# Performance work log

Hardware: AMD Instinct MI355X
Metric: run time of the kernel (lower is better)

The kernel has to match this reference:

```python
import jax, jax.numpy as jnp
import numpy as np


def conv1x1(x, w, b):
    # x: [B,Cin,H,W], w: [Cout,Cin], b: [Cout]
    return jnp.einsum('bchw,oc->bohw', x, w) + b[None, :, None, None]


def setup_inputs() -> dict:
    key = jax.random.key(0)
    ks = jax.random.split(key, 10)
    B, Cm, C, H, W = 4, 6, 64, 64, 64
    map1 = jax.random.normal(ks[0], (B, Cm, H, W), jnp.float32)
    map2 = jax.random.normal(ks[1], (B, Cm, H, W), jnp.float32)
    feature_map = jax.random.normal(ks[2], (B, C, H, W), jnp.float32)
    # 1x1 conv params (kaiming-ish scale)
    wb = jax.random.normal(ks[3], (Cm, Cm), jnp.float32) / np.sqrt(Cm)
    bb = jnp.zeros((Cm,), jnp.float32)
    wc = jax.random.normal(ks[4], (Cm, Cm), jnp.float32) / np.sqrt(Cm)
    bc = jnp.zeros((Cm,), jnp.float32)
    wd = jax.random.normal(ks[5], (C, C), jnp.float32) / np.sqrt(C)
    bd = jnp.zeros((C,), jnp.float32)
    alpha = jnp.zeros((1,), jnp.float32)
    return {"map1": map1, "map2": map2, "feature_map": feature_map,
            "wb": wb, "bb": bb, "wc": wc, "bc": bc, "wd": wd, "bd": bd,
            "alpha": alpha}


def reference(map1, map2, feature_map, wb, bb, wc, bc, wd, bd, alpha):
    B, _, H, W = map1.shape
    N = H * W
    # conv1x1 projections, flatten spatial
    feat_b = conv1x1(map1, wb, bb).reshape(B, -1, N).transpose(0, 2, 1)  # [B,N,6]
    feat_c = conv1x1(map2, wc, bc).reshape(B, -1, N)                      # [B,6,N]
    attention_s = jax.nn.softmax(jnp.einsum('bnc,bcm->bnm', feat_b, feat_c), axis=-1)  # [B,N,N]
    feat_d = conv1x1(feature_map, wd, bd).reshape(B, -1, N)               # [B,C,N]
    # bmm with attention_s^T: out[b,c,n] = sum_m feat_d[b,c,m] * attn[b,n,m]
    feat_e = jnp.einsum('bcm,bnm->bcn', feat_d, attention_s).reshape(B, -1, H, W)
    return alpha * feat_e + feature_map
```

## Files before the change

kernel.cpp:

```cpp
#include <hip/hip_runtime.h>
#include <hip/hip_bf16.h>
#include <math.h>


#define BATCH 4
#define CMAP  6
#define CH    64
#define NSP   4096
#define TN    64
#define PSTR  72

typedef __attribute__((ext_vector_type(8))) short short8;
typedef __attribute__((ext_vector_type(4))) float f32x4;

#if __has_builtin(__builtin_amdgcn_exp2f)
#define EXP2(x) __builtin_amdgcn_exp2f(x)
#else
#define EXP2(x) exp2f(x)
#endif

__device__ __forceinline__ unsigned f2bf(float f) {
    unsigned u = __float_as_uint(f);
    return (u + 0x7fffu + ((u >> 16) & 1u)) >> 16;
}

#define INVLN2 1.44269504088896f
#define SHIFT_BF16 0xC238u
#define ONE_BF16   0x3F80u


__global__ void proj_kernel(const float* __restrict__ map1, const float* __restrict__ map2,
                            const float* __restrict__ fm,
                            const float* __restrict__ wb, const float* __restrict__ bb,
                            const float* __restrict__ wc, const float* __restrict__ bc,
                            const float* __restrict__ wd, const float* __restrict__ bd,
                            unsigned short* __restrict__ featq8,
                            unsigned short* __restrict__ featk8,
                            unsigned short* __restrict__ featdf)
{
    __shared__ unsigned short vfrag[2048];

    const int b    = blockIdx.z;
    const int half = blockIdx.y;
    const int lane = threadIdx.x & 63;
    const int og   = threadIdx.x >> 6;
    const int n    = blockIdx.x * 64 + lane;

    const int ht = lane >> 5;
    const int mm = lane & 31;
    const int q4 = mm >> 3, jj = mm & 7;
    const int cb_local = og >> 1;
    float vals[CH];
#pragma unroll
    for (int c = 0; c < CH; ++c)
        vals[c] = fm[(size_t)(b*CH + c)*NSP + n];
#pragma unroll
    for (int oi = 0; oi < 8; ++oi) {
        const int o = half*32 + og*8 + oi;
        float a = bd[o];
#pragma unroll
        for (int c = 0; c < CH; ++c)
            a = fmaf(vals[c], wd[o*CH + c], a);
        const int r = (og & 1)*8 + oi;
        vfrag[(ht*2 + cb_local)*512 + (q4*16 + r)*8 + jj] = (unsigned short)f2bf(a);
    }

    if (half == 0 && og == 0) {
        float v1[CMAP], v2[CMAP];
#pragma unroll
        for (int c = 0; c < CMAP; ++c) {
            v1[c] = map1[(size_t)(b*CMAP + c)*NSP + n];
            v2[c] = map2[(size_t)(b*CMAP + c)*NSP + n];
        }
        unsigned qv[CMAP], kv[CMAP];
#pragma unroll
        for (int o = 0; o < CMAP; ++o) {
            float a1 = bb[o], a2 = bc[o];
#pragma unroll
            for (int c = 0; c < CMAP; ++c) {
                a1 = fmaf(v1[c], wb[o*CMAP + c], a1);
                a2 = fmaf(v2[c], wc[o*CMAP + c], a2);
            }
            qv[o] = f2bf(a1 * INVLN2);
            kv[o] = f2bf(a2);
        }
        uint4 qw, kw;
        qw.x = qv[0] | (qv[1] << 16);
        qw.y = qv[2] | (qv[3] << 16);
        qw.z = qv[4] | (qv[5] << 16);
        qw.w = SHIFT_BF16;
        kw.x = kv[0] | (kv[1] << 16);
        kw.y = kv[2] | (kv[3] << 16);
        kw.z = kv[4] | (kv[5] << 16);
        kw.w = ONE_BF16;
        *(uint4*)&featq8[(size_t)(b*NSP + n)*8] = qw;
        *(uint4*)&featk8[(size_t)(b*NSP + n)*8] = kw;
    }

    __syncthreads();

    {
        const int tt = threadIdx.x;
        const uint4 d = *(const uint4*)&vfrag[tt*8];
        const int ht2 = tt >> 7, inner = tt & 127;
        const size_t off = (((size_t)(b*128 + blockIdx.x*2 + ht2)*4) + half*2)*512
                         + (size_t)inner*8;
        *(uint4*)&featdf[off] = d;
    }
}

__global__ __launch_bounds__(256, 2)
void attn_kernel(const unsigned short* __restrict__ featq8,
                 const unsigned short* __restrict__ featk8,
                 const unsigned short* __restrict__ featdf,
                 const float* __restrict__ fm, const float* __restrict__ alpha_p,
                 float* __restrict__ out)
{
    __shared__ unsigned short p_scr[2][4][16*PSTR];
    __shared__ float l_scr[4][16];

    const int b    = blockIdx.z;
    const int chh  = blockIdx.y;
    const int t    = threadIdx.x;
    const int lane = t & 63, w = t >> 6;
    const int row16 = lane & 15, quad = lane >> 4;
    const int n0w  = blockIdx.x * 64 + w * 16;

    short8 qf = {0,0,0,0,0,0,0,0};
    if (quad == 0)
        qf = *(const short8*)&featq8[(size_t)(b*NSP + n0w + row16)*8];

    const unsigned short* kbase = featk8 + ((size_t)b*NSP + row16)*8 + quad*8;
    const unsigned short* vfb = featdf + ((size_t)b*128*4)*512 + lane*8;
    const int cb0 = chh*2, cb1 = chh*2 + 1;

    const f32x4 zf = {0.f,0.f,0.f,0.f};
    f32x4 acc0 = zf, acc1 = zf;
    float lacc = 0.f;
    const int prow = row16 * PSTR;

#define PAM_DO(pwp, mb, sv)                                                     \
    {                                                                           \
        const float p0 = EXP2(sv[0]), p1 = EXP2(sv[1]);                         \
        const float p2 = EXP2(sv[2]), p3 = EXP2(sv[3]);                         \
        lacc += (p0 + p1) + (p2 + p3);                                          \
        uint2 pp;                                                               \
        pp.x = __builtin_amdgcn_perm(__float_as_uint(p1), __float_as_uint(p0), 0x07060302u); \
        pp.y = __builtin_amdgcn_perm(__float_as_uint(p3), __float_as_uint(p2), 0x07060302u); \
        *(uint2*)((pwp) + (mb)*16) = pp;                                        \
    }

    short8 k0 = *(const short8*)(kbase +  0*8);
    short8 k1 = *(const short8*)(kbase + 16*8);
    short8 k2 = *(const short8*)(kbase + 32*8);
    short8 k3 = *(const short8*)(kbase + 48*8);
    short8 vn0 = *(const short8*)(vfb + (size_t)(0*4 + cb0)*512);
    short8 vn1 = *(const short8*)(vfb + (size_t)(1*4 + cb0)*512);
    short8 vn2 = *(const short8*)(vfb + (size_t)(0*4 + cb1)*512);
    short8 vn3 = *(const short8*)(vfb + (size_t)(1*4 + cb1)*512);

    f32x4 s0 = __builtin_amdgcn_mfma_f32_16x16x32_bf16(k0, qf, zf, 0, 0, 0);
    f32x4 s1 = __builtin_amdgcn_mfma_f32_16x16x32_bf16(k1, qf, zf, 0, 0, 0);
    f32x4 s2 = __builtin_amdgcn_mfma_f32_16x16x32_bf16(k2, qf, zf, 0, 0, 0);
    f32x4 s3 = __builtin_amdgcn_mfma_f32_16x16x32_bf16(k3, qf, zf, 0, 0, 0);
    {
        unsigned short* pw = &p_scr[0][w][prow + quad*4];
        PAM_DO(pw, 0, s0) PAM_DO(pw, 1, s1) PAM_DO(pw, 2, s2) PAM_DO(pw, 3, s3)
    }
    k0 = *(const short8*)(kbase + (64 +  0)*8);
    k1 = *(const short8*)(kbase + (64 + 16)*8);
    k2 = *(const short8*)(kbase + (64 + 32)*8);
    k3 = *(const short8*)(kbase + (64 + 48)*8);
    short8 vv0 = vn0, vv1 = vn1, vv2 = vn2, vv3 = vn3;
    vn0 = *(const short8*)(vfb + (size_t)((2 + 0)*4 + cb0)*512);
    vn1 = *(const short8*)(vfb + (size_t)((2 + 1)*4 + cb0)*512);
    vn2 = *(const short8*)(vfb + (size_t)((2 + 0)*4 + cb1)*512);
    vn3 = *(const short8*)(vfb + (size_t)((2 + 1)*4 + cb1)*512);

#pragma unroll 2
    for (int tc = 1; tc < NSP/TN; ++tc) {
        const int par = tc & 1;

        s0 = __builtin_amdgcn_mfma_f32_16x16x32_bf16(k0, qf, zf, 0, 0, 0);
        s1 = __builtin_amdgcn_mfma_f32_16x16x32_bf16(k1, qf, zf, 0, 0, 0);
        s2 = __builtin_amdgcn_mfma_f32_16x16x32_bf16(k2, qf, zf, 0, 0, 0);
        s3 = __builtin_amdgcn_mfma_f32_16x16x32_bf16(k3, qf, zf, 0, 0, 0);

        const int kn = ((tc + 1) & (NSP/TN - 1)) * TN;
        const short8 k0n = *(const short8*)(kbase + (kn +  0)*8);
        const short8 k1n = *(const short8*)(kbase + (kn + 16)*8);
        const short8 k2n = *(const short8*)(kbase + (kn + 32)*8);
        const short8 k3n = *(const short8*)(kbase + (kn + 48)*8);

        const unsigned short* pr = &p_scr[par ^ 1][w][prow + quad*8];
        const short8 a0 = *(const short8*)pr;
        const short8 a1 = *(const short8*)(pr + 32);

        {
            unsigned short* pw = &p_scr[par][w][prow + quad*4];
            PAM_DO(pw, 0, s0) PAM_DO(pw, 1, s1) PAM_DO(pw, 2, s2) PAM_DO(pw, 3, s3)
        }

        acc0 = __builtin_amdgcn_mfma_f32_16x16x32_bf16(a0, vv0, acc0, 0, 0, 0);
        acc0 = __builtin_amdgcn_mfma_f32_16x16x32_bf16(a1, vv1, acc0, 0, 0, 0);
        acc1 = __builtin_amdgcn_mfma_f32_16x16x32_bf16(a0, vv2, acc1, 0, 0, 0);
        acc1 = __builtin_amdgcn_mfma_f32_16x16x32_bf16(a1, vv3, acc1, 0, 0, 0);

        vv0 = vn0; vv1 = vn1; vv2 = vn2; vv3 = vn3;
        const int vt = (tc + 1) & (NSP/TN - 1);
        vn0 = *(const short8*)(vfb + (size_t)((vt*2 + 0)*4 + cb0)*512);
        vn1 = *(const short8*)(vfb + (size_t)((vt*2 + 1)*4 + cb0)*512);
        vn2 = *(const short8*)(vfb + (size_t)((vt*2 + 0)*4 + cb1)*512);
        vn3 = *(const short8*)(vfb + (size_t)((vt*2 + 1)*4 + cb1)*512);

        k0 = k0n; k1 = k1n; k2 = k2n; k3 = k3n;
    }

    {
        const unsigned short* pr = &p_scr[1][w][prow + quad*8];
        const short8 a0 = *(const short8*)pr;
        const short8 a1 = *(const short8*)(pr + 32);
        acc0 = __builtin_amdgcn_mfma_f32_16x16x32_bf16(a0, vv0, acc0, 0, 0, 0);
        acc0 = __builtin_amdgcn_mfma_f32_16x16x32_bf16(a1, vv1, acc0, 0, 0, 0);
        acc1 = __builtin_amdgcn_mfma_f32_16x16x32_bf16(a0, vv2, acc1, 0, 0, 0);
        acc1 = __builtin_amdgcn_mfma_f32_16x16x32_bf16(a1, vv3, acc1, 0, 0, 0);
    }
#undef PAM_DO

    lacc += __shfl_xor(lacc, 16);
    lacc += __shfl_xor(lacc, 32);
    if (quad == 0) l_scr[w][row16] = lacc;
    const float4 lv = *(const float4*)&l_scr[w][quad*4];

    const float alpha = alpha_p[0];
    const float c0 = alpha / (lv.x + 1e-30f);
    const float c1 = alpha / (lv.y + 1e-30f);
    const float c2 = alpha / (lv.z + 1e-30f);
    const float c3 = alpha / (lv.w + 1e-30f);
#pragma unroll
    for (int cb = 0; cb < 2; ++cb) {
        const int ch = chh*32 + cb*16 + row16;
        const size_t base = (size_t)(b*CH + ch)*NSP + n0w + quad*4;
        const float4 f = *(const float4*)&fm[base];
        const f32x4 a = cb ? acc1 : acc0;
        float4 o;
        o.x = fmaf(c0, a[0], f.x);
        o.y = fmaf(c1, a[1], f.y);
        o.z = fmaf(c2, a[2], f.z);
        o.w = fmaf(c3, a[3], f.w);
        *(float4*)&out[base] = o;
    }
}

extern "C" void kernel_launch(void* const* d_in, const int* in_sizes, int n_in,
                              void* d_out, int out_size, void* d_ws, size_t ws_size,
                              hipStream_t stream)
{
    const float* map1  = (const float*)d_in[0];
    const float* map2  = (const float*)d_in[1];
    const float* fm    = (const float*)d_in[2];
    const float* wb    = (const float*)d_in[3];
    const float* bb    = (const float*)d_in[4];
    const float* wc    = (const float*)d_in[5];
    const float* bc    = (const float*)d_in[6];
    const float* wd    = (const float*)d_in[7];
    const float* bd    = (const float*)d_in[8];
    const float* alpha = (const float*)d_in[9];
    float* out = (float*)d_out;

    unsigned short* featq8 = (unsigned short*)d_ws;
    unsigned short* featk8 = featq8 + (size_t)BATCH*NSP*8;
    unsigned short* featdf = featk8 + (size_t)BATCH*NSP*8;

    proj_kernel<<<dim3(NSP/64, 2, BATCH), 256, 0, stream>>>(
        map1, map2, fm, wb, bb, wc, bc, wd, bd, featq8, featk8, featdf);
    attn_kernel<<<dim3(NSP/64, 2, BATCH), 256, 0, stream>>>(
        featq8, featk8, featdf, fm, alpha, out);
}
```

Before: 122.6 us.

## Compute softmax row sums via MFMA with ones and deepen QK pipeline

Replaces the per-lane VALU accumulation of exponentials and the shuffle/LDS reduction with two extra MFMAs per tile that multiply the bf16 P fragments by a ones vector, giving row sums directly in accumulator layout. It also restructures the software pipeline so QK scores for tile i are computed while tile i-1's scores are exponentiated, giving the MFMA latency a full iteration to hide. The row sum now comes from the bf16-rounded probabilities, which matches the numerator but changes rounding, and the extra MFMAs and live registers add matrix-unit work and register pressure.

```diff
diff --git a/kernel.cpp b/kernel.cpp
--- a/kernel.cpp
+++ b/kernel.cpp
@@ -8,6 +8,7 @@
 #define CH    64
 #define NSP   4096
 #define TN    64
+#define NT    (NSP/TN)
 #define PSTR  72
 
 typedef __attribute__((ext_vector_type(8))) short short8;
@@ -117,7 +118,6 @@
                  float* __restrict__ out)
 {
     __shared__ unsigned short p_scr[2][4][16*PSTR];
-    __shared__ float l_scr[4][16];
 
     const int b    = blockIdx.z;
     const int chh  = blockIdx.y;
@@ -130,92 +130,107 @@
     if (quad == 0)
         qf = *(const short8*)&featq8[(size_t)(b*NSP + n0w + row16)*8];
 
+    const short8 onesb = {(short)ONE_BF16,(short)ONE_BF16,(short)ONE_BF16,(short)ONE_BF16,
+                          (short)ONE_BF16,(short)ONE_BF16,(short)ONE_BF16,(short)ONE_BF16};
+
     const unsigned short* kbase = featk8 + ((size_t)b*NSP + row16)*8 + quad*8;
     const unsigned short* vfb = featdf + ((size_t)b*128*4)*512 + lane*8;
     const int cb0 = chh*2, cb1 = chh*2 + 1;
 
     const f32x4 zf = {0.f,0.f,0.f,0.f};
-    f32x4 acc0 = zf, acc1 = zf;
-    float lacc = 0.f;
+    f32x4 acc0 = zf, acc1 = zf, accL = zf;
     const int prow = row16 * PSTR;
 
 #define PAM_DO(pwp, mb, sv)                                                     \
     {                                                                           \
         const float p0 = EXP2(sv[0]), p1 = EXP2(sv[1]);                         \
         const float p2 = EXP2(sv[2]), p3 = EXP2(sv[3]);                         \
-        lacc += (p0 + p1) + (p2 + p3);                                          \
         uint2 pp;                                                               \
         pp.x = __builtin_amdgcn_perm(__float_as_uint(p1), __float_as_uint(p0), 0x07060302u); \
         pp.y = __builtin_amdgcn_perm(__float_as_uint(p3), __float_as_uint(p2), 0x07060302u); \
         *(uint2*)((pwp) + (mb)*16) = pp;                                        \
     }
 
-    short8 k0 = *(const short8*)(kbase +  0*8);
-    short8 k1 = *(const short8*)(kbase + 16*8);
-    short8 k2 = *(const short8*)(kbase + 32*8);
-    short8 k3 = *(const short8*)(kbase + 48*8);
-    short8 vn0 = *(const short8*)(vfb + (size_t)(0*4 + cb0)*512);
-    short8 vn1 = *(const short8*)(vfb + (size_t)(1*4 + cb0)*512);
-    short8 vn2 = *(const short8*)(vfb + (size_t)(0*4 + cb1)*512);
-    short8 vn3 = *(const short8*)(vfb + (size_t)(1*4 + cb1)*512);
-
-    f32x4 s0 = __builtin_amdgcn_mfma_f32_16x16x32_bf16(k0, qf, zf, 0, 0, 0);
-    f32x4 s1 = __builtin_amdgcn_mfma_f32_16x16x32_bf16(k1, qf, zf, 0, 0, 0);
-    f32x4 s2 = __builtin_amdgcn_mfma_f32_16x16x32_bf16(k2, qf, zf, 0, 0, 0);
-    f32x4 s3 = __builtin_amdgcn_mfma_f32_16x16x32_bf16(k3, qf, zf, 0, 0, 0);
-    {
+#define LOADK(dst, mt)                                                          \
+    dst##0 = *(const short8*)(kbase + ((mt)*TN +  0)*8);                        \
+    dst##1 = *(const short8*)(kbase + ((mt)*TN + 16)*8);                        \
+    dst##2 = *(const short8*)(kbase + ((mt)*TN + 32)*8);                        \
+    dst##3 = *(const short8*)(kbase + ((mt)*TN + 48)*8);
+
+#define LOADV(dst, vt)                                                          \
+    dst##0 = *(const short8*)(vfb + (size_t)(((vt)*2 + 0)*4 + cb0)*512);        \
+    dst##1 = *(const short8*)(vfb + (size_t)(((vt)*2 + 1)*4 + cb0)*512);        \
+    dst##2 = *(const short8*)(vfb + (size_t)(((vt)*2 + 0)*4 + cb1)*512);        \
+    dst##3 = *(const short8*)(vfb + (size_t)(((vt)*2 + 1)*4 + cb1)*512);
+
+    short8 kc0, kc1, kc2, kc3, kn0, kn1, kn2, kn3;
+    short8 vv0, vv1, vv2, vv3, vn0, vn1, vn2, vn3;
+    f32x4 sp0, sp1, sp2, sp3;
+
+    LOADK(kc, 0)
+    LOADV(vv, 0)
+    LOADV(vn, 1)
+
+    {
+        f32x4 a0 = __builtin_amdgcn_mfma_f32_16x16x32_bf16(kc0, qf, zf, 0, 0, 0);
+        f32x4 a1 = __builtin_amdgcn_mfma_f32_16x16x32_bf16(kc1, qf, zf, 0, 0, 0);
+        f32x4 a2 = __builtin_amdgcn_mfma_f32_16x16x32_bf16(kc2, qf, zf, 0, 0, 0);
+        f32x4 a3 = __builtin_amdgcn_mfma_f32_16x16x32_bf16(kc3, qf, zf, 0, 0, 0);
+        LOADK(kc, 1)
         unsigned short* pw = &p_scr[0][w][prow + quad*4];
-        PAM_DO(pw, 0, s0) PAM_DO(pw, 1, s1) PAM_DO(pw, 2, s2) PAM_DO(pw, 3, s3)
-    }
-    k0 = *(const short8*)(kbase + (64 +  0)*8);
-    k1 = *(const short8*)(kbase + (64 + 16)*8);
-    k2 = *(const short8*)(kbase + (64 + 32)*8);
-    k3 = *(const short8*)(kbase + (64 + 48)*8);
-    short8 vv0 = vn0, vv1 = vn1, vv2 = vn2, vv3 = vn3;
-    vn0 = *(const short8*)(vfb + (size_t)((2 + 0)*4 + cb0)*512);
-    vn1 = *(const short8*)(vfb + (size_t)((2 + 1)*4 + cb0)*512);
-    vn2 = *(const short8*)(vfb + (size_t)((2 + 0)*4 + cb1)*512);
-    vn3 = *(const short8*)(vfb + (size_t)((2 + 1)*4 + cb1)*512);
+        PAM_DO(pw, 0, a0) PAM_DO(pw, 1, a1) PAM_DO(pw, 2, a2) PAM_DO(pw, 3, a3)
+    }
+    sp0 = __builtin_amdgcn_mfma_f32_16x16x32_bf16(kc0, qf, zf, 0, 0, 0);
+    sp1 = __builtin_amdgcn_mfma_f32_16x16x32_bf16(kc1, qf, zf, 0, 0, 0);
+    sp2 = __builtin_amdgcn_mfma_f32_16x16x32_bf16(kc2, qf, zf, 0, 0, 0);
+    sp3 = __builtin_amdgcn_mfma_f32_16x16x32_bf16(kc3, qf, zf, 0, 0, 0);
+    LOADK(kc, 2)
 
 #pragma unroll 2
-    for (int tc = 1; tc < NSP/TN; ++tc) {
-        const int par = tc & 1;
-
-        s0 = __builtin_amdgcn_mfma_f32_16x16x32_bf16(k0, qf, zf, 0, 0, 0);
-        s1 = __builtin_amdgcn_mfma_f32_16x16x32_bf16(k1, qf, zf, 0, 0, 0);
-        s2 = __builtin_amdgcn_mfma_f32_16x16x32_bf16(k2, qf, zf, 0, 0, 0);
-        s3 = __builtin_amdgcn_mfma_f32_16x16x32_bf16(k3, qf, zf, 0, 0, 0);
-
-        const int kn = ((tc + 1) & (NSP/TN - 1)) * TN;
-        const short8 k0n = *(const short8*)(kbase + (kn +  0)*8);
-        const short8 k1n = *(const short8*)(kbase + (kn + 16)*8);
-        const short8 k2n = *(const short8*)(kbase + (kn + 32)*8);
-        const short8 k3n = *(const short8*)(kbase + (kn + 48)*8);
-
-        const unsigned short* pr = &p_scr[par ^ 1][w][prow + quad*8];
+    for (int i = 2; i < NT; ++i) {
+        const f32x4 t0 = __builtin_amdgcn_mfma_f32_16x16x32_bf16(kc0, qf, zf, 0, 0, 0);
+        const f32x4 t1 = __builtin_amdgcn_mfma_f32_16x16x32_bf16(kc1, qf, zf, 0, 0, 0);
+        const f32x4 t2 = __builtin_amdgcn_mfma_f32_16x16x32_bf16(kc2, qf, zf, 0, 0, 0);
+        const f32x4 t3 = __builtin_amdgcn_mfma_f32_16x16x32_bf16(kc3, qf, zf, 0, 0, 0);
+
+        const unsigned short* pr = &p_scr[i & 1][w][prow + quad*8];
         const short8 a0 = *(const short8*)pr;
         const short8 a1 = *(const short8*)(pr + 32);
 
+        LOADK(kn, i + 1)
+
         {
-            unsigned short* pw = &p_scr[par][w][prow + quad*4];
-            PAM_DO(pw, 0, s0) PAM_DO(pw, 1, s1) PAM_DO(pw, 2, s2) PAM_DO(pw, 3, s3)
+            unsigned short* pw = &p_scr[(i + 1) & 1][w][prow + quad*4];
+            PAM_DO(pw, 0, sp0) PAM_DO(pw, 1, sp1) PAM_DO(pw, 2, sp2) PAM_DO(pw, 3, sp3)
         }
 
         acc0 = __builtin_amdgcn_mfma_f32_16x16x32_bf16(a0, vv0, acc0, 0, 0, 0);
         acc0 = __builtin_amdgcn_mfma_f32_16x16x32_bf16(a1, vv1, acc0, 0, 0, 0);
         acc1 = __builtin_amdgcn_mfma_f32_16x16x32_bf16(a0, vv2, acc1, 0, 0, 0);
         acc1 = __builtin_amdgcn_mfma_f32_16x16x32_bf16(a1, vv3, acc1, 0, 0, 0);
+        accL = __builtin_amdgcn_mfma_f32_16x16x32_bf16(a0, onesb, accL, 0, 0, 0);
+        accL = __builtin_amdgcn_mfma_f32_16x16x32_bf16(a1, onesb, accL, 0, 0, 0);
 
         vv0 = vn0; vv1 = vn1; vv2 = vn2; vv3 = vn3;
-        const int vt = (tc + 1) & (NSP/TN - 1);
-        vn0 = *(const short8*)(vfb + (size_t)((vt*2 + 0)*4 + cb0)*512);
-        vn1 = *(const short8*)(vfb + (size_t)((vt*2 + 1)*4 + cb0)*512);
-        vn2 = *(const short8*)(vfb + (size_t)((vt*2 + 0)*4 + cb1)*512);
-        vn3 = *(const short8*)(vfb + (size_t)((vt*2 + 1)*4 + cb1)*512);
-
-        k0 = k0n; k1 = k1n; k2 = k2n; k3 = k3n;
-    }
-
+        LOADV(vn, i)
+        kc0 = kn0; kc1 = kn1; kc2 = kn2; kc3 = kn3;
+        sp0 = t0; sp1 = t1; sp2 = t2; sp3 = t3;
+    }
+
+    {
+        const unsigned short* pr = &p_scr[0][w][prow + quad*8];
+        const short8 a0 = *(const short8*)pr;
+        const short8 a1 = *(const short8*)(pr + 32);
+        unsigned short* pw = &p_scr[1][w][prow + quad*4];
+        PAM_DO(pw, 0, sp0) PAM_DO(pw, 1, sp1) PAM_DO(pw, 2, sp2) PAM_DO(pw, 3, sp3)
+        acc0 = __builtin_amdgcn_mfma_f32_16x16x32_bf16(a0, vv0, acc0, 0, 0, 0);
+        acc0 = __builtin_amdgcn_mfma_f32_16x16x32_bf16(a1, vv1, acc0, 0, 0, 0);
+        acc1 = __builtin_amdgcn_mfma_f32_16x16x32_bf16(a0, vv2, acc1, 0, 0, 0);
+        acc1 = __builtin_amdgcn_mfma_f32_16x16x32_bf16(a1, vv3, acc1, 0, 0, 0);
+        accL = __builtin_amdgcn_mfma_f32_16x16x32_bf16(a0, onesb, accL, 0, 0, 0);
+        accL = __builtin_amdgcn_mfma_f32_16x16x32_bf16(a1, onesb, accL, 0, 0, 0);
+        vv0 = vn0; vv1 = vn1; vv2 = vn2; vv3 = vn3;
+    }
     {
         const unsigned short* pr = &p_scr[1][w][prow + quad*8];
         const short8 a0 = *(const short8*)pr;
@@ -224,19 +239,18 @@
         acc0 = __builtin_amdgcn_mfma_f32_16x16x32_bf16(a1, vv1, acc0, 0, 0, 0);
         acc1 = __builtin_amdgcn_mfma_f32_16x16x32_bf16(a0, vv2, acc1, 0, 0, 0);
         acc1 = __builtin_amdgcn_mfma_f32_16x16x32_bf16(a1, vv3, acc1, 0, 0, 0);
+        accL = __builtin_amdgcn_mfma_f32_16x16x32_bf16(a0, onesb, accL, 0, 0, 0);
+        accL = __builtin_amdgcn_mfma_f32_16x16x32_bf16(a1, onesb, accL, 0, 0, 0);
     }
 #undef PAM_DO
-
-    lacc += __shfl_xor(lacc, 16);
-    lacc += __shfl_xor(lacc, 32);
-    if (quad == 0) l_scr[w][row16] = lacc;
-    const float4 lv = *(const float4*)&l_scr[w][quad*4];
+#undef LOADK
+#undef LOADV
 
     const float alpha = alpha_p[0];
-    const float c0 = alpha / (lv.x + 1e-30f);
-    const float c1 = alpha / (lv.y + 1e-30f);
-    const float c2 = alpha / (lv.z + 1e-30f);
-    const float c3 = alpha / (lv.w + 1e-30f);
+    const float c0 = alpha / (accL[0] + 1e-30f);
+    const float c1 = alpha / (accL[1] + 1e-30f);
+    const float c2 = alpha / (accL[2] + 1e-30f);
+    const float c3 = alpha / (accL[3] + 1e-30f);
 #pragma unroll
     for (int cb = 0; cb < 2; ++cb) {
         const int ch = chh*32 + cb*16 + row16;
```

Result: no change. 123.2 us (+0.5%).
